# Kernel optimization log

Measured on AMD Instinct MI355X. Metric: run time of the kernel, lower is better.

Reference implementation:

```python
import jax, jax.numpy as jnp
import numpy as np

GAMMA = 0.1   # gl.gamma
BIG = 1e10    # stand-in for +inf in the DP border (keeps grads NaN-free)


def _softdtw(D, gamma=GAMMA):
    """Soft-DTW value for a batch of cost matrices D: [B, T, T] -> [B].
    R[i,j] = D[i,j] + softmin_gamma(R[i-1,j-1], R[i-1,j], R[i,j-1]).
    Vectorized over the batch; sequential DP over rows (outer scan) and
    columns (inner scan), matching the reference recurrence exactly.
    """
    B, T, _ = D.shape
    dt = D.dtype
    # R[0, :] = [0, inf, inf, ...]  (length T+1, padded border)
    prev = jnp.concatenate([jnp.zeros((B, 1), dt), jnp.full((B, T), BIG, dt)], axis=1)

    def col_step(r_left, xs):
        d, r_diag, r_up = xs  # each [B]
        stacked = jnp.stack([r_diag, r_up, r_left])  # [3, B]
        r = d - gamma * jax.nn.logsumexp(-stacked / gamma, axis=0)
        return r, r

    def row_step(prev_row, d_row):  # prev_row [B, T+1], d_row [B, T]
        xs = (d_row.T, prev_row[:, :-1].T, prev_row[:, 1:].T)  # each [T, B]
        _, rows = jax.lax.scan(col_step, jnp.full((B,), BIG, dt), xs)  # [T, B]
        new_row = jnp.concatenate([jnp.full((B, 1), BIG, dt), rows.T], axis=1)
        return new_row, None

    final_row, _ = jax.lax.scan(row_step, prev, jnp.swapaxes(D, 0, 1))
    return final_row[:, -1]  # R[T, T]


def setup_inputs() -> dict:
    key = jax.random.key(0)
    n_class, n_support, n_query, t, c = 20, 5, 25, 32, 2048
    n = n_class * (n_support + n_query)
    inp = jax.random.normal(key, (n, t, c), jnp.float32)
    # episode labels, grouped per class (as produced by an episodic sampler)
    target = jnp.repeat(jnp.arange(n_class, dtype=jnp.int32), n_support + n_query)
    return {"inp": inp, "target": target, "n_support": n_support, "n_class": n_class}


def reference(inp, target, n_support, n_class):
    n, t, c = inp.shape
    per_class = n // n_class
    n_query = per_class - n_support

    # group samples by class (stable sort == torch.nonzero(target.eq(c)) ordering)
    order = jnp.argsort(target, stable=True)
    grouped = inp[order].reshape(n_class, per_class, t, c)
    z_proto = grouped[:, :n_support].mean(axis=1)                 # [m, t, c]
    zq = grouped[:, n_support:].reshape(n_class * n_query, t, c)  # [nq, t, c]

    # pairwise squared-Euclidean frame costs (no [nq*m, t, c] expansion)
    x2 = jnp.sum(zq * zq, axis=-1)          # [nq, t]
    y2 = jnp.sum(z_proto * z_proto, axis=-1)  # [m, t]
    xy = jnp.einsum('nic,mjc->nmij', zq, z_proto)  # [nq, m, t, t]
    cost_xy = x2[:, None, :, None] + y2[None, :, None, :] - 2.0 * xy
    nq, m = cost_xy.shape[:2]
    d_xy = _softdtw(cost_xy.reshape(nq * m, t, t)).reshape(nq, m)

    # normalization terms: D(x,x), D(y,y)
    cxx = x2[:, :, None] + x2[:, None, :] - 2.0 * jnp.einsum('nic,njc->nij', zq, zq)
    cyy = y2[:, :, None] + y2[:, None, :] - 2.0 * jnp.einsum('mic,mjc->mij', z_proto, z_proto)
    d_xx = _softdtw(cxx)  # [nq]
    d_yy = _softdtw(cyy)  # [m]
    dist = d_xy - 0.5 * (d_xx[:, None] + d_yy[None, :])  # [nq, m]

    log_p_y = jax.nn.log_softmax(-dist, axis=1).reshape(n_class, n_query, n_class)
    tgt = jnp.broadcast_to(jnp.arange(n_class)[:, None, None], (n_class, n_query, 1))
    batch_loss = -jnp.take_along_axis(log_p_y, tgt, axis=2).reshape(-1)
    loss_val = batch_loss.mean()
    y_hat = jnp.argmax(log_p_y, axis=2)
    acc_val = (y_hat == tgt[..., 0]).astype(jnp.float32).mean()
    return loss_val, acc_val, batch_loss
```

## Files before the change

kernel.cpp:

```cpp
#include <hip/hip_runtime.h>

#define T 32
#define C 2048
#define NTOT 600
#define NCLASS 20
#define NSUP 5
#define PER 30
#define NQPC 25
#define NQ 500
#define NQROWS (NQ * T)
#define NPROWS (NCLASS * T)
#define GAMMA 0.1f
#define INVG 10.0f
#define BIG 1e10f
#define NMM (NQ * NCLASS + NQ + NCLASS)
#define GEMM_BLKS 625
#define SYRK_BLKS_PAD 136
#define STAGE_BLKS_A 2000
#define STAGE_BLKS_B 80
#define LDS_PITCH 33

typedef __fp16 half8 __attribute__((ext_vector_type(8)));
typedef __fp16 half4 __attribute__((ext_vector_type(4)));
typedef float f32x4 __attribute__((ext_vector_type(4)));

__global__ __launch_bounds__(640) void sort_kernel(const int* __restrict__ target,
                                                   int* __restrict__ order,
                                                   int* __restrict__ qsrc) {
    __shared__ int tgt[NTOT];
    __shared__ int offs[NCLASS];
    __shared__ int ordl[NTOT];
    int tid = threadIdx.x;
    if (tid < NTOT) tgt[tid] = target[tid];
    __syncthreads();
    if (tid < NCLASS) {
        int o = 0;
        for (int i = 0; i < NTOT; i++) o += (tgt[i] < tid) ? 1 : 0;
        offs[tid] = o;
    }
    __syncthreads();
    if (tid < NTOT) {
        int c = tgt[tid];
        int rank = 0;
        for (int k = 0; k < NTOT; k++) rank += (k < tid && tgt[k] == c) ? 1 : 0;
        ordl[offs[c] + rank] = tid;
    }
    __syncthreads();
    if (tid < NTOT) order[tid] = ordl[tid];
    if (tid < NQ) qsrc[tid] = ordl[(tid / NQPC) * PER + NSUP + (tid % NQPC)];
}

__global__ __launch_bounds__(256) void stage_kernel(const float* __restrict__ inp,
                                                    const int* __restrict__ qsrc,
                                                    const int* __restrict__ order,
                                                    half8* __restrict__ Ah,
                                                    half8* __restrict__ Bh) {
    __shared__ half8 lds[4][16][LDS_PITCH];
    int tid = threadIdx.x;
    int lane = tid & 63, w = tid >> 6;
    int bid = blockIdx.x;
    bool isA = bid < STAGE_BLKS_A;
    int b = isA ? bid : bid - STAGE_BLKS_A;
    int rowblk = b >> 1, half = b & 1;
    int row0 = rowblk * 16;
    int colbase = half * 1024 + w * 256;
    int nrows = isA ? NQROWS : NPROWS;
    half8* dst = isA ? Ah : Bh;
    if (isA) {
#pragma unroll
        for (int rr = 0; rr < 16; rr++) {
            int rg = row0 + rr;
            const float* src = inp + (size_t)qsrc[rg >> 5] * (T * C) +
                               (size_t)(rg & 31) * C + colbase + lane * 4;
            float4 v = *(const float4*)src;
            half4 hv = {(__fp16)v.x, (__fp16)v.y, (__fp16)v.z, (__fp16)v.w};
            ((half4*)&lds[w][rr][0])[lane] = hv;
        }
    } else {
#pragma unroll
        for (int rr = 0; rr < 16; rr++) {
            int rg = row0 + rr;
            int cls = rg >> 5, trow = rg & 31;
            const float* base = inp + (size_t)trow * C + colbase + lane * 4;
            float4 a = *(const float4*)(base + (size_t)order[cls * PER + 0] * (T * C));
            float4 b4 = *(const float4*)(base + (size_t)order[cls * PER + 1] * (T * C));
            float4 c = *(const float4*)(base + (size_t)order[cls * PER + 2] * (T * C));
            float4 d = *(const float4*)(base + (size_t)order[cls * PER + 3] * (T * C));
            float4 e = *(const float4*)(base + (size_t)order[cls * PER + 4] * (T * C));
            float4 m;
            m.x = (a.x + b4.x + c.x + d.x + e.x) * 0.2f;
            m.y = (a.y + b4.y + c.y + d.y + e.y) * 0.2f;
            m.z = (a.z + b4.z + c.z + d.z + e.z) * 0.2f;
            m.w = (a.w + b4.w + c.w + d.w + e.w) * 0.2f;
            half4 hv = {(__fp16)m.x, (__fp16)m.y, (__fp16)m.z, (__fp16)m.w};
            ((half4*)&lds[w][rr][0])[lane] = hv;
        }
    }
    __syncthreads();
    int chunkbase = half * 128 + w * 32;
#pragma unroll
    for (int c = 0; c < 8; c++) {
        int idx = c * 64 + lane;
        int ch = idx >> 4, row = idx & 15;
        dst[(size_t)(chunkbase + ch) * nrows + row0 + row] = lds[w][row][ch];
    }
}

__global__ __launch_bounds__(256) void gemm_syrk_kernel(const half8* __restrict__ Ah,
                                                        const half8* __restrict__ Bh,
                                                        float* __restrict__ xy,
                                                        float* __restrict__ gxx,
                                                        float* __restrict__ gyy) {
    int tid = threadIdx.x, lane = tid & 63, wid = tid >> 6;
    int o = blockIdx.x;
    int g = lane >> 4, r = lane & 15;
    if (o < SYRK_BLKS_PAD) {
        int ww = o * 4 + wid;
        if (ww >= NQ + NCLASS) return;
        const half8* hi;
        int nrows, row0;
        float* outp;
        if (ww < NQ) {
            hi = Ah; nrows = NQROWS; row0 = ww * 32;
            outp = gxx + (size_t)ww * (T * T);
        } else {
            hi = Bh; nrows = NPROWS; row0 = (ww - NQ) * 32;
            outp = gyy + (size_t)(ww - NQ) * (T * T);
        }
        f32x4 acc[2][2];
        f32x4 zero = {0.f, 0.f, 0.f, 0.f};
        acc[0][0] = zero; acc[0][1] = zero; acc[1][0] = zero; acc[1][1] = zero;
        for (int t = 0; t < C / 32; t++) {
            size_t base = (size_t)(t * 4 + g) * nrows + row0 + r;
            half8 h0 = hi[base], h1 = hi[base + 16];
            acc[0][0] = __builtin_amdgcn_mfma_f32_16x16x32_f16(h0, h0, acc[0][0], 0, 0, 0);
            acc[0][1] = __builtin_amdgcn_mfma_f32_16x16x32_f16(h0, h1, acc[0][1], 0, 0, 0);
            acc[1][0] = __builtin_amdgcn_mfma_f32_16x16x32_f16(h1, h0, acc[1][0], 0, 0, 0);
            acc[1][1] = __builtin_amdgcn_mfma_f32_16x16x32_f16(h1, h1, acc[1][1], 0, 0, 0);
        }
#pragma unroll
        for (int mi = 0; mi < 2; mi++)
#pragma unroll
            for (int ni = 0; ni < 2; ni++)
#pragma unroll
                for (int j = 0; j < 4; j++)
                    outp[(mi * 16 + g * 4 + j) * T + ni * 16 + r] = acc[mi][ni][j];
        return;
    }
    int oo = o - SYRK_BLKS_PAD;
    int xcd = oo & 7, slot = oo >> 3;
    int v = (xcd < 1 ? xcd * 79 : 79 + (xcd - 1) * 78) + slot;
    int bm = v / 5, bn = v % 5;
    int wr = wid >> 1, wc = wid & 1;
    int m0 = bm * 128 + wr * 64, n0 = bn * 128 + wc * 64;
    const half8* pA = Ah + (size_t)g * NQROWS + m0 + r;
    const half8* pB = Bh + (size_t)g * NPROWS + n0 + r;
    f32x4 acc[4][4];
    f32x4 zero = {0.f, 0.f, 0.f, 0.f};
#pragma unroll
    for (int mi = 0; mi < 4; mi++)
#pragma unroll
        for (int ni = 0; ni < 4; ni++) acc[mi][ni] = zero;
#pragma unroll 2
    for (int t = 0; t < C / 32; t++) {
        half8 ah[4], bh[4];
#pragma unroll
        for (int i = 0; i < 4; i++) {
            ah[i] = pA[i * 16];
            bh[i] = pB[i * 16];
        }
        pA += 4 * NQROWS;
        pB += 4 * NPROWS;
#pragma unroll
        for (int mi = 0; mi < 4; mi++)
#pragma unroll
            for (int ni = 0; ni < 4; ni++)
                acc[mi][ni] = __builtin_amdgcn_mfma_f32_16x16x32_f16(ah[mi], bh[ni], acc[mi][ni], 0, 0, 0);
    }
    int orow = m0 + g * 4;
    int ocol = n0 + r;
#pragma unroll
    for (int mi = 0; mi < 4; mi++)
#pragma unroll
        for (int ni = 0; ni < 4; ni++)
#pragma unroll
            for (int j = 0; j < 4; j++)
                xy[(size_t)(orow + mi * 16 + j) * NPROWS + ocol + ni * 16] = acc[mi][ni][j];
}

__global__ void diag_kernel(const float* __restrict__ gxx, const float* __restrict__ gyy,
                            float* __restrict__ x2, float* __restrict__ y2) {
    int i = blockIdx.x * 256 + threadIdx.x;
    if (i < NQROWS) {
        x2[i] = gxx[(size_t)(i >> 5) * (T * T) + (i & 31) * (T + 1)];
    } else if (i < NQROWS + NPROWS) {
        int j = i - NQROWS;
        y2[j] = gyy[(size_t)(j >> 5) * (T * T) + (j & 31) * (T + 1)];
    }
}

__global__ __launch_bounds__(256) void softdtw_wave_kernel(
        const float* __restrict__ xy, const float* __restrict__ gxx,
        const float* __restrict__ gyy, const float* __restrict__ x2,
        const float* __restrict__ y2, float* __restrict__ dxy,
        float* __restrict__ dxx, float* __restrict__ dyy) {
    int tid = threadIdx.x;
    int j = tid & 31;
    int mm = blockIdx.x * 8 + (tid >> 5);
    bool valid = mm < NMM;
    int mmc = valid ? mm : 0;
    const float* rterm;
    const float* cterm;
    const float* cptr;
    int cstride;
    float* outp;
    if (mmc < NQ * NCLASS) {
        int q = mmc / NCLASS, m = mmc % NCLASS;
        rterm = x2 + q * T;
        cterm = y2 + m * T;
        cptr = xy + (size_t)(q * T) * NPROWS + m * T;
        cstride = NPROWS;
        outp = dxy + mmc;
    } else if (mmc < NQ * NCLASS + NQ) {
        int i = mmc - NQ * NCLASS;
        rterm = x2 + i * T;
        cterm = rterm;
        cptr = gxx + (size_t)i * (T * T);
        cstride = T;
        outp = dxx + i;
    } else {
        int i = mmc - NQ * NCLASS - NQ;
        rterm = y2 + i * T;
        cterm = rterm;
        cptr = gyy + (size_t)i * (T * T);
        cstride = T;
        outp = dyy + i;
    }
    float cjv = cterm[j];
    float xreg = rterm[j];
    float my_prev = BIG, my_prev2 = BIG;
    int ip = 0 - j; ip = ip < 0 ? 0 : (ip > 31 ? 31 : ip);
    float nxt_xy = cptr[(size_t)ip * cstride + j];
    for (int k = 0; k < 63; k++) {
        float cur_xy = nxt_xy;
        int in = k + 1 - j; in = in < 0 ? 0 : (in > 31 ? 31 : in);
        nxt_xy = cptr[(size_t)in * cstride + j];
        float lp = __shfl_up(my_prev, 1, 32);
        float dg = __shfl_up(my_prev2, 1, 32);
        if (j == 0) { lp = BIG; dg = (k == 0) ? 0.f : BIG; }
        float up = my_prev;
        int i = k - j;
        float ai = __shfl(xreg, i & 31, 32);
        float d = ai + cjv - 2.0f * cur_xy;
        float mn = fminf(dg, fminf(up, lp));
        float ssum = __expf((mn - dg) * INVG) + __expf((mn - up) * INVG) +
                     __expf((mn - lp) * INVG);
        float r = d + mn - GAMMA * __logf(ssum);
        bool active = (i >= 0) && (i < 32);
        my_prev2 = my_prev;
        my_prev = active ? r : my_prev;
    }
    if (j == 31 && valid) *outp = my_prev;
}

__global__ __launch_bounds__(512) void finalize_kernel(const float* __restrict__ dxy,
                                                       const float* __restrict__ dxx,
                                                       const float* __restrict__ dyy,
                                                       float* __restrict__ out) {
    __shared__ float sl[512];
    __shared__ float sa[512];
    int q = threadIdx.x;
    float bl = 0.f, fl = 0.f;
    if (q < NQ) {
        float dxxq = dxx[q];
        int cq = q / NQPC;
        float dd[NCLASS];
#pragma unroll
        for (int m = 0; m < NCLASS; m++)
            dd[m] = dxy[q * NCLASS + m] - 0.5f * (dxxq + dyy[m]);
        float best = dd[0];
        int bi = 0;
#pragma unroll
        for (int m = 1; m < NCLASS; m++) {
            if (dd[m] < best) { best = dd[m]; bi = m; }
        }
        float s = 0.f;
        float dcq = dd[0];
#pragma unroll
        for (int m = 0; m < NCLASS; m++) {
            s += __expf(best - dd[m]);
            if (m == cq) dcq = dd[m];
        }
        float lse = __logf(s) - best;
        bl = dcq + lse;
        out[2 + q] = bl;
        fl = (bi == cq) ? 1.f : 0.f;
    }
    sl[threadIdx.x] = bl;
    sa[threadIdx.x] = fl;
    __syncthreads();
    for (int off = 256; off; off >>= 1) {
        if (threadIdx.x < off) {
            sl[threadIdx.x] += sl[threadIdx.x + off];
            sa[threadIdx.x] += sa[threadIdx.x + off];
        }
        __syncthreads();
    }
    if (threadIdx.x == 0) {
        out[0] = sl[0] / (float)NQ;
        out[1] = sa[0] / (float)NQ;
    }
}

extern "C" void kernel_launch(void* const* d_in, const int* in_sizes, int n_in,
                              void* d_out, int out_size, void* d_ws, size_t ws_size,
                              hipStream_t stream) {
    const float* inp = (const float*)d_in[0];
    const int* target = (const int*)d_in[1];
    float* out = (float*)d_out;
    char* ws = (char*)d_ws;

    size_t off = 0;
    auto carve = [&](size_t bytes) {
        void* p = ws + off;
        off = (off + bytes + 255) & ~(size_t)255;
        return p;
    };
    int* order = (int*)carve(NTOT * sizeof(int));
    int* qsrc = (int*)carve(NQ * sizeof(int));
    float* x2 = (float*)carve((size_t)NQROWS * sizeof(float));
    float* y2 = (float*)carve((size_t)NPROWS * sizeof(float));
    float* xy = (float*)carve((size_t)NQROWS * NPROWS * sizeof(float));
    float* gxx = (float*)carve((size_t)NQ * T * T * sizeof(float));
    float* gyy = (float*)carve((size_t)NCLASS * T * T * sizeof(float));
    float* dxy = (float*)carve((size_t)NQ * NCLASS * sizeof(float));
    float* dxx = (float*)carve((size_t)NQ * sizeof(float));
    float* dyy = (float*)carve((size_t)NCLASS * sizeof(float));
    half8* Ah = (half8*)carve((size_t)(C / 8) * NQROWS * 16);
    half8* Bh = (half8*)carve((size_t)(C / 8) * NPROWS * 16);
    (void)ws_size;

    sort_kernel<<<1, 640, 0, stream>>>(target, order, qsrc);
    stage_kernel<<<STAGE_BLKS_A + STAGE_BLKS_B, 256, 0, stream>>>(inp, qsrc, order, Ah, Bh);
    gemm_syrk_kernel<<<SYRK_BLKS_PAD + GEMM_BLKS, 256, 0, stream>>>(Ah, Bh, xy, gxx, gyy);
    diag_kernel<<<(NQROWS + NPROWS + 255) / 256, 256, 0, stream>>>(gxx, gyy, x2, y2);
    softdtw_wave_kernel<<<(NMM + 7) / 8, 256, 0, stream>>>(xy, gxx, gyy, x2, y2, dxy, dxx, dyy);
    finalize_kernel<<<1, 512, 0, stream>>>(dxy, dxx, dyy, out);
}
```

Before: 180.4 us.

## Stage all samples per-sample layout, move query gather into GEMM loads

The stage kernel now converts every one of the 600 input samples to fp16 in a per-sample chunked layout, so it no longer gathers through qsrc. It also no longer depends on the sort kernel's query indices. The GEMM and SYRK kernels resolve the query permutation themselves by indexing Ah through qsrc for each 32-row sample. This removes the dependent index load from the staging path, at the cost of staging 100 extra support samples (20% more conversion traffic) and scattering A-operand reads across samples.

```diff
diff --git a/kernel.cpp b/kernel.cpp
--- a/kernel.cpp
+++ b/kernel.cpp
@@ -16,7 +16,8 @@
 #define NMM (NQ * NCLASS + NQ + NCLASS)
 #define GEMM_BLKS 625
 #define SYRK_BLKS_PAD 136
-#define STAGE_BLKS_A 2000
+#define SAMP_STRIDE 8192
+#define STAGE_BLKS_A 2400
 #define STAGE_BLKS_B 80
 #define LDS_PITCH 33
 
@@ -51,7 +52,6 @@
 }
 
 __global__ __launch_bounds__(256) void stage_kernel(const float* __restrict__ inp,
-                                                    const int* __restrict__ qsrc,
                                                     const int* __restrict__ order,
                                                     half8* __restrict__ Ah,
                                                     half8* __restrict__ Bh) {
@@ -64,17 +64,24 @@
     int rowblk = b >> 1, half = b & 1;
     int row0 = rowblk * 16;
     int colbase = half * 1024 + w * 256;
-    int nrows = isA ? NQROWS : NPROWS;
-    half8* dst = isA ? Ah : Bh;
     if (isA) {
+        int sample = row0 >> 5, rowin0 = row0 & 31;
+        const float* sbase = inp + (size_t)sample * (T * C) + (size_t)rowin0 * C +
+                             colbase + lane * 4;
 #pragma unroll
         for (int rr = 0; rr < 16; rr++) {
-            int rg = row0 + rr;
-            const float* src = inp + (size_t)qsrc[rg >> 5] * (T * C) +
-                               (size_t)(rg & 31) * C + colbase + lane * 4;
-            float4 v = *(const float4*)src;
+            float4 v = *(const float4*)(sbase + (size_t)rr * C);
             half4 hv = {(__fp16)v.x, (__fp16)v.y, (__fp16)v.z, (__fp16)v.w};
             ((half4*)&lds[w][rr][0])[lane] = hv;
+        }
+        __syncthreads();
+        int chunkbase = half * 128 + w * 32;
+        half8* dst = Ah + (size_t)sample * SAMP_STRIDE + rowin0;
+#pragma unroll
+        for (int c = 0; c < 8; c++) {
+            int idx = c * 64 + lane;
+            int ch = idx >> 4, row = idx & 15;
+            dst[(size_t)(chunkbase + ch) * 32 + row] = lds[w][row][ch];
         }
     } else {
 #pragma unroll
@@ -95,19 +102,20 @@
             half4 hv = {(__fp16)m.x, (__fp16)m.y, (__fp16)m.z, (__fp16)m.w};
             ((half4*)&lds[w][rr][0])[lane] = hv;
         }
-    }
-    __syncthreads();
-    int chunkbase = half * 128 + w * 32;
-#pragma unroll
-    for (int c = 0; c < 8; c++) {
-        int idx = c * 64 + lane;
-        int ch = idx >> 4, row = idx & 15;
-        dst[(size_t)(chunkbase + ch) * nrows + row0 + row] = lds[w][row][ch];
+        __syncthreads();
+        int chunkbase = half * 128 + w * 32;
+#pragma unroll
+        for (int c = 0; c < 8; c++) {
+            int idx = c * 64 + lane;
+            int ch = idx >> 4, row = idx & 15;
+            Bh[(size_t)(chunkbase + ch) * NPROWS + row0 + row] = lds[w][row][ch];
+        }
     }
 }
 
 __global__ __launch_bounds__(256) void gemm_syrk_kernel(const half8* __restrict__ Ah,
                                                         const half8* __restrict__ Bh,
+                                                        const int* __restrict__ qsrc,
                                                         float* __restrict__ xy,
                                                         float* __restrict__ gxx,
                                                         float* __restrict__ gyy) {
@@ -117,34 +125,46 @@
     if (o < SYRK_BLKS_PAD) {
         int ww = o * 4 + wid;
         if (ww >= NQ + NCLASS) return;
-        const half8* hi;
-        int nrows, row0;
-        float* outp;
-        if (ww < NQ) {
-            hi = Ah; nrows = NQROWS; row0 = ww * 32;
-            outp = gxx + (size_t)ww * (T * T);
-        } else {
-            hi = Bh; nrows = NPROWS; row0 = (ww - NQ) * 32;
-            outp = gyy + (size_t)(ww - NQ) * (T * T);
-        }
         f32x4 acc[2][2];
         f32x4 zero = {0.f, 0.f, 0.f, 0.f};
         acc[0][0] = zero; acc[0][1] = zero; acc[1][0] = zero; acc[1][1] = zero;
-        for (int t = 0; t < C / 32; t++) {
-            size_t base = (size_t)(t * 4 + g) * nrows + row0 + r;
-            half8 h0 = hi[base], h1 = hi[base + 16];
-            acc[0][0] = __builtin_amdgcn_mfma_f32_16x16x32_f16(h0, h0, acc[0][0], 0, 0, 0);
-            acc[0][1] = __builtin_amdgcn_mfma_f32_16x16x32_f16(h0, h1, acc[0][1], 0, 0, 0);
-            acc[1][0] = __builtin_amdgcn_mfma_f32_16x16x32_f16(h1, h0, acc[1][0], 0, 0, 0);
-            acc[1][1] = __builtin_amdgcn_mfma_f32_16x16x32_f16(h1, h1, acc[1][1], 0, 0, 0);
-        }
-#pragma unroll
-        for (int mi = 0; mi < 2; mi++)
-#pragma unroll
-            for (int ni = 0; ni < 2; ni++)
-#pragma unroll
-                for (int j = 0; j < 4; j++)
-                    outp[(mi * 16 + g * 4 + j) * T + ni * 16 + r] = acc[mi][ni][j];
+        if (ww < NQ) {
+            const half8* p = Ah + (size_t)qsrc[ww] * SAMP_STRIDE + g * 32 + r;
+            float* outp = gxx + (size_t)ww * (T * T);
+            for (int t = 0; t < C / 32; t++) {
+                half8 h0 = p[0], h1 = p[16];
+                p += 128;
+                acc[0][0] = __builtin_amdgcn_mfma_f32_16x16x32_f16(h0, h0, acc[0][0], 0, 0, 0);
+                acc[0][1] = __builtin_amdgcn_mfma_f32_16x16x32_f16(h0, h1, acc[0][1], 0, 0, 0);
+                acc[1][0] = __builtin_amdgcn_mfma_f32_16x16x32_f16(h1, h0, acc[1][0], 0, 0, 0);
+                acc[1][1] = __builtin_amdgcn_mfma_f32_16x16x32_f16(h1, h1, acc[1][1], 0, 0, 0);
+            }
+#pragma unroll
+            for (int mi = 0; mi < 2; mi++)
+#pragma unroll
+                for (int ni = 0; ni < 2; ni++)
+#pragma unroll
+                    for (int j = 0; j < 4; j++)
+                        outp[(mi * 16 + g * 4 + j) * T + ni * 16 + r] = acc[mi][ni][j];
+        } else {
+            int row0 = (ww - NQ) * 32;
+            float* outp = gyy + (size_t)(ww - NQ) * (T * T);
+            for (int t = 0; t < C / 32; t++) {
+                size_t base = (size_t)(t * 4 + g) * NPROWS + row0 + r;
+                half8 h0 = Bh[base], h1 = Bh[base + 16];
+                acc[0][0] = __builtin_amdgcn_mfma_f32_16x16x32_f16(h0, h0, acc[0][0], 0, 0, 0);
+                acc[0][1] = __builtin_amdgcn_mfma_f32_16x16x32_f16(h0, h1, acc[0][1], 0, 0, 0);
+                acc[1][0] = __builtin_amdgcn_mfma_f32_16x16x32_f16(h1, h0, acc[1][0], 0, 0, 0);
+                acc[1][1] = __builtin_amdgcn_mfma_f32_16x16x32_f16(h1, h1, acc[1][1], 0, 0, 0);
+            }
+#pragma unroll
+            for (int mi = 0; mi < 2; mi++)
+#pragma unroll
+                for (int ni = 0; ni < 2; ni++)
+#pragma unroll
+                    for (int j = 0; j < 4; j++)
+                        outp[(mi * 16 + g * 4 + j) * T + ni * 16 + r] = acc[mi][ni][j];
+        }
         return;
     }
     int oo = o - SYRK_BLKS_PAD;
@@ -153,7 +173,9 @@
     int bm = v / 5, bn = v % 5;
     int wr = wid >> 1, wc = wid & 1;
     int m0 = bm * 128 + wr * 64, n0 = bn * 128 + wc * 64;
-    const half8* pA = Ah + (size_t)g * NQROWS + m0 + r;
+    int q0 = m0 >> 5;
+    const half8* pA0 = Ah + (size_t)qsrc[q0] * SAMP_STRIDE + g * 32 + r;
+    const half8* pA1 = Ah + (size_t)qsrc[q0 + 1] * SAMP_STRIDE + g * 32 + r;
     const half8* pB = Bh + (size_t)g * NPROWS + n0 + r;
     f32x4 acc[4][4];
     f32x4 zero = {0.f, 0.f, 0.f, 0.f};
@@ -164,12 +186,14 @@
 #pragma unroll 2
     for (int t = 0; t < C / 32; t++) {
         half8 ah[4], bh[4];
-#pragma unroll
-        for (int i = 0; i < 4; i++) {
-            ah[i] = pA[i * 16];
-            bh[i] = pB[i * 16];
-        }
-        pA += 4 * NQROWS;
+        ah[0] = pA0[0];
+        ah[1] = pA0[16];
+        ah[2] = pA1[0];
+        ah[3] = pA1[16];
+#pragma unroll
+        for (int i = 0; i < 4; i++) bh[i] = pB[i * 16];
+        pA0 += 128;
+        pA1 += 128;
         pB += 4 * NPROWS;
 #pragma unroll
         for (int mi = 0; mi < 4; mi++)
@@ -336,13 +360,13 @@
     float* dxy = (float*)carve((size_t)NQ * NCLASS * sizeof(float));
     float* dxx = (float*)carve((size_t)NQ * sizeof(float));
     float* dyy = (float*)carve((size_t)NCLASS * sizeof(float));
-    half8* Ah = (half8*)carve((size_t)(C / 8) * NQROWS * 16);
+    half8* Ah = (half8*)carve((size_t)NTOT * SAMP_STRIDE * 16);
     half8* Bh = (half8*)carve((size_t)(C / 8) * NPROWS * 16);
     (void)ws_size;
 
     sort_kernel<<<1, 640, 0, stream>>>(target, order, qsrc);
-    stage_kernel<<<STAGE_BLKS_A + STAGE_BLKS_B, 256, 0, stream>>>(inp, qsrc, order, Ah, Bh);
-    gemm_syrk_kernel<<<SYRK_BLKS_PAD + GEMM_BLKS, 256, 0, stream>>>(Ah, Bh, xy, gxx, gyy);
+    stage_kernel<<<STAGE_BLKS_A + STAGE_BLKS_B, 256, 0, stream>>>(inp, order, Ah, Bh);
+    gemm_syrk_kernel<<<SYRK_BLKS_PAD + GEMM_BLKS, 256, 0, stream>>>(Ah, Bh, qsrc, xy, gxx, gyy);
     diag_kernel<<<(NQROWS + NPROWS + 255) / 256, 256, 0, stream>>>(gxx, gyy, x2, y2);
     softdtw_wave_kernel<<<(NMM + 7) / 8, 256, 0, stream>>>(xy, gxx, gyy, x2, y2, dxy, dxx, dyy);
     finalize_kernel<<<1, 512, 0, stream>>>(dxy, dxx, dyy, out);
```

New measurement: 178.1 us. About the same (-1.3%).
